# Performance work log

Hardware: AMD Instinct MI355X
Metric: run time of the kernel (lower is better)

Reference implementation:

```python
import jax, jax.numpy as jnp
import numpy as np
from jax import lax

L, B, H, Z, V = 64, 32, 256, 256, 32000  # steps, max_ast_depth, hidden=units, latent, vocab


def setup_inputs() -> dict:
    key = jax.random.key(0)
    ks = jax.random.split(key, 32)
    p = lambda i, shape: jax.random.normal(ks[i], shape, dtype=jnp.float32) * 0.05
    inp = {
        "nodes": jax.random.randint(ks[0], (L, B), 0, V),
        "edges": jax.random.randint(ks[1], (L, B), 0, 2) > 0,
        "enc_init": jax.random.normal(ks[2], (B, H), dtype=jnp.float32) * 0.001,
        "eps": jax.random.normal(ks[3], (B, Z), dtype=jnp.float32),
        "emb": p(4, (V, H)),
    }
    for j, n in enumerate(["enc_c", "enc_s", "dec_c", "dec_s"]):
        inp[n + "_Wih"] = p(5 + 4 * j, (3 * H, H))
        inp[n + "_Whh"] = p(6 + 4 * j, (3 * H, H))
        inp[n + "_bih"] = p(7 + 4 * j, (3 * H,))
        inp[n + "_bhh"] = p(8 + 4 * j, (3 * H,))
    inp["W_mean"] = p(21, (Z, H)); inp["b_mean"] = p(22, (Z,))
    inp["W_logv"] = p(23, (Z, H)); inp["b_logv"] = p(24, (Z,))
    inp["W_l2h"] = p(25, (H, Z)); inp["b_l2h"] = p(26, (H,))
    inp["W_voc"] = p(27, (V, H)); inp["b_voc"] = p(28, (V,))
    return inp


def _gru_cell(Wih, Whh, bih, bhh, x, h):
    # torch.nn.GRU single-layer cell; x, h: [B, H]
    gi = x @ Wih.T + bih
    gh = h @ Whh.T + bhh
    ir, iz, inn = jnp.split(gi, 3, axis=-1)
    hr, hz, hn = jnp.split(gh, 3, axis=-1)
    r = jax.nn.sigmoid(ir + hr)
    zg = jax.nn.sigmoid(iz + hz)
    n = jnp.tanh(inn + r * hn)
    return (1.0 - zg) * n + zg * h


def _tree_rnn(pc, ps, emb_nodes, edges, h0):
    # emb_nodes: [L, B, H], edges: [L, B] bool, h0: [B, H]
    # each step runs child & sibling GRUs on the SAME state, selects per node by edge
    def step(h, xe):
        x, e = xe
        hc = _gru_cell(*pc, x, h)
        hs = _gru_cell(*ps, x, h)
        h_new = jnp.where(e[:, None], hc, hs)
        return h_new, h_new  # 1-layer GRU, seq_len 1: output == new state
    h_final, outs = lax.scan(step, h0, (emb_nodes, edges))
    return outs, h_final  # outs: [L, B, H]


def reference(nodes, edges, enc_init, eps, emb,
              enc_c_Wih, enc_c_Whh, enc_c_bih, enc_c_bhh,
              enc_s_Wih, enc_s_Whh, enc_s_bih, enc_s_bhh,
              dec_c_Wih, dec_c_Whh, dec_c_bih, dec_c_bhh,
              dec_s_Wih, dec_s_Whh, dec_s_bih, dec_s_bhh,
              W_mean, b_mean, W_logv, b_logv, W_l2h, b_l2h, W_voc, b_voc):
    x = emb[nodes]  # [L, B, H]
    _, h_enc = _tree_rnn((enc_c_Wih, enc_c_Whh, enc_c_bih, enc_c_bhh),
                         (enc_s_Wih, enc_s_Whh, enc_s_bih, enc_s_bhh),
                         x, edges, enc_init)
    mean = h_enc @ W_mean.T + b_mean          # [B, Z]
    logv = h_enc @ W_logv.T + b_logv
    z = eps * jnp.exp(0.5 * logv) + mean      # reparameterization
    h0 = z @ W_l2h.T + b_l2h                  # decoder initial state [B, H]
    outs, _ = _tree_rnn((dec_c_Wih, dec_c_Whh, dec_c_bih, dec_c_bhh),
                        (dec_s_Wih, dec_s_Whh, dec_s_bih, dec_s_bhh),
                        x, edges, h0)         # [L, B, H]
    logits = outs @ W_voc.T + b_voc           # [L, B, V]
    logp = jax.nn.log_softmax(logits, axis=-1)
    return logp, mean, logv, z
```

## Files before the change

### kernel.cpp

```cpp
#include <hip/hip_runtime.h>
#include <stdint.h>

typedef unsigned short u16;
typedef unsigned int u32;

#define L_STEPS 64
#define B_SZ 32
#define H_SZ 256
#define Z_SZ 256
#define V_SZ 32000
#define H2 128
#define G3H 768

typedef _Float16 h2_t __attribute__((ext_vector_type(2)));
typedef _Float16 f16x8 __attribute__((ext_vector_type(8)));
typedef float f32x4 __attribute__((ext_vector_type(4)));

#define WHH2_OFF   0
#define WIH2_OFF   393216
#define WM2_OFF    786432
#define WLV2_OFF   819200
#define WL2H2_OFF  851968
#define GI2_OFF    884736
#define OUTS2_OFF  4030464
#define W16_OFF    4292608
#define WS_NEEDED  ((size_t)(W16_OFF + 4096000) * 4)

#define OUT_MEAN_OFF  65536000
#define OUT_LOGV_OFF  65544192
#define OUT_Z_OFF     65552384

__device__ __forceinline__ float fdot2(h2_t a, h2_t b, float c){
#if __has_builtin(__builtin_amdgcn_fdot2)
  return __builtin_amdgcn_fdot2(a, b, c, false);
#else
  return c + (float)a.x*(float)b.x + (float)a.y*(float)b.y;
#endif
}
__device__ __forceinline__ float sigm(float x){ return 1.f/(1.f + __expf(-x)); }

struct PackTArgs { const float2* src[11]; int n_h2[11]; int dstoff[11]; };

__global__ __launch_bounds__(256) void k_packt(PackTArgs p, h2_t* wsh){
  int m = blockIdx.y;
  int r = blockIdx.x*256 + threadIdx.x;
  if (r >= p.n_h2[m]) return;
  int row = r >> 7, k2 = r & 127;
  float2 f = p.src[m][r];
  h2_t h; h.x = (_Float16)f.x; h.y = (_Float16)f.y;
  int off = (((row>>6)*32 + (k2>>2))*64 + (row&63))*4 + (k2&3);
  wsh[p.dstoff[m] + off] = h;
}

__global__ __launch_bounds__(256) void k_packv(const float2* __restrict__ src,
                                               h2_t* __restrict__ dst, int total){
  int idx = blockIdx.x*256 + threadIdx.x;
  if (idx >= total) return;
  float2 f = src[idx];
  h2_t h; h.x = (_Float16)f.x; h.y = (_Float16)f.y;
  dst[idx] = h;
}

struct GiArgs { const float* bih[4]; };

__global__ __launch_bounds__(256) void k_gi(const int* __restrict__ nodes,
                                            const float* __restrict__ emb,
                                            const h2_t* __restrict__ wih2,
                                            GiArgs ga, h2_t* __restrict__ gi2){
  int l = blockIdx.x, g = blockIdx.y, t = threadIdx.x;
  __shared__ __align__(16) h2_t x2[B_SZ*132];
  #pragma unroll
  for (int it=0; it<16; ++it){
    int lin = it*256 + t;
    int bb = lin >> 7, k2 = lin & 127;
    int node = nodes[l*B_SZ + bb];
    float2 f = ((const float2*)(emb + (size_t)node*H_SZ))[k2];
    h2_t r; r.x=(_Float16)f.x; r.y=(_Float16)f.y;
    x2[bb*132 + k2] = r;
  }
  __syncthreads();
  const float* bih = ga.bih[g];
  for (int jc=0; jc<3; ++jc){
    int j = jc*256 + t;
    float acc[32];
    #pragma unroll
    for (int bb=0;bb<32;bb++) acc[bb]=0.f;
    const float4* Wv = (const float4*)wih2 + (size_t)g*24576 + (j>>6)*2048 + (j&63);
    #pragma unroll 2
    for (int kb=0;kb<32;kb++){
      union{float4 f; h2_t h[4];} w4;
      w4.f = Wv[kb*64];
      #pragma unroll
      for (int kc=0;kc<4;kc++){
        h2_t w = w4.h[kc];
        int k2 = kb*4 + kc;
        #pragma unroll
        for (int bb=0;bb<32;bb++) acc[bb] = fdot2(x2[bb*132+k2], w, acc[bb]);
      }
    }
    float bvv = bih[j];
    int base = (g*2048 + l*B_SZ)*384 + (j>>1);
    #pragma unroll
    for (int bb=0;bb<32;bb++){
      float own = acc[bb] + bvv;
      float oth = __shfl_xor(own, 1, 64);
      if (!(t&1)){
        h2_t r; r.x=(_Float16)own; r.y=(_Float16)oth;
        gi2[base + bb*384] = r;
      }
    }
  }
}

struct ScanArgs {
  const float* bhh[4];
  const float* b_mean; const float* b_logv; const float* b_l2h;
  const float* enc_init; const float* eps;
};

__global__ __launch_bounds__(768) void k_scan(const int* __restrict__ edges, ScanArgs sa,
                                              const h2_t* __restrict__ wsh,
                                              h2_t* __restrict__ outs2,
                                              float* __restrict__ out){
  int b = blockIdx.x, t = threadIdx.x;
  int i = t & 255, gate = t >> 8;
  int lane = t & 63, rb = t >> 6;
  __shared__ float h_lds[H_SZ];
  __shared__ __align__(16) h2_t hs2[H2];
  __shared__ float g_lds[512];
  __shared__ float s_bhh[4*G3H];
  __shared__ int s_edge[L_STEPS];
  const _Float16* gi_all = (const _Float16*)(wsh + GI2_OFF);

  if (t < H_SZ) h_lds[t] = sa.enc_init[b*H_SZ + t];
  if (t < L_STEPS) s_edge[t] = edges[t*B_SZ + b];
  #pragma unroll
  for (int m=0;m<4;m++) s_bhh[m*G3H + t] = sa.bhh[m][t];
  __syncthreads();
  if (t < H2){ h2_t r; r.x=(_Float16)h_lds[2*t]; r.y=(_Float16)h_lds[2*t+1]; hs2[t]=r; }
  __syncthreads();

  const float4* hsv = (const float4*)hs2;

  for (int ph=0; ph<2; ++ph){
    for (int l=0; l<L_STEPS; ++l){
      int e = s_edge[l];
      int gsel = (ph ? 2 : 0) + (e ? 0 : 1);
      float gi0=0.f, gi1=0.f, gi2v=0.f;
      if (t < H_SZ){
        const _Float16* gr = gi_all + (size_t)(gsel*2048 + l*B_SZ + b)*G3H;
        gi0  = (float)gr[i];
        gi1  = (float)gr[256+i];
        gi2v = (float)gr[512+i];
      }
      float bv = s_bhh[gsel*G3H + t];
      const float4* Wv = (const float4*)wsh + (size_t)gsel*24576 + rb*2048 + lane;
      float a0=0.f,a1=0.f,a2=0.f,a3=0.f;
      #pragma unroll 8
      for (int kb=0;kb<32;kb++){
        union{float4 f; h2_t h[4];} w, x;
        w.f = Wv[kb*64];
        x.f = hsv[kb];
        a0 = fdot2(x.h[0], w.h[0], a0);
        a1 = fdot2(x.h[1], w.h[1], a1);
        a2 = fdot2(x.h[2], w.h[2], a2);
        a3 = fdot2(x.h[3], w.h[3], a3);
      }
      float acc = (a0+a1)+(a2+a3) + bv;
      if (gate) g_lds[(gate-1)*256 + i] = acc;
      __syncthreads();
      if (t < H_SZ){
        float r = sigm(gi0 + acc);
        float z = sigm(gi1 + g_lds[i]);
        float n = tanhf(gi2v + r*g_lds[256+i]);
        float hn = (1.f - z)*n + z*h_lds[i];
        h_lds[i] = hn;
        float ho = __shfl_xor(hn, 1, 64);
        if (!(i & 1)){
          h2_t pk; pk.x=(_Float16)hn; pk.y=(_Float16)ho;
          hs2[i>>1] = pk;
          if (ph) outs2[(l*B_SZ + b)*H2 + (i>>1)] = pk;
        }
      }
      __syncthreads();
    }

    if (ph == 0){
      if (t < H_SZ){
        const float4* WmV = (const float4*)(wsh + WM2_OFF)  + (t>>6)*2048 + (t&63);
        const float4* WlV = (const float4*)(wsh + WLV2_OFF) + (t>>6)*2048 + (t&63);
        float m0=0.f,m1=0.f,m2=0.f,m3=0.f, l0=0.f,l1=0.f,l2=0.f,l3=0.f;
        #pragma unroll 8
        for (int kb=0;kb<32;kb++){
          union{float4 f; h2_t h[4];} wm, wl, x;
          x.f  = hsv[kb];
          wm.f = WmV[kb*64];
          wl.f = WlV[kb*64];
          m0=fdot2(x.h[0],wm.h[0],m0); m1=fdot2(x.h[1],wm.h[1],m1);
          m2=fdot2(x.h[2],wm.h[2],m2); m3=fdot2(x.h[3],wm.h[3],m3);
          l0=fdot2(x.h[0],wl.h[0],l0); l1=fdot2(x.h[1],wl.h[1],l1);
          l2=fdot2(x.h[2],wl.h[2],l2); l3=fdot2(x.h[3],wl.h[3],l3);
        }
        float am = (m0+m1)+(m2+m3) + sa.b_mean[t];
        float al = (l0+l1)+(l2+l3) + sa.b_logv[t];
        float zv = sa.eps[b*Z_SZ + t] * __expf(0.5f*al) + am;
        out[OUT_MEAN_OFF + b*Z_SZ + t] = am;
        out[OUT_LOGV_OFF + b*Z_SZ + t] = al;
        out[OUT_Z_OFF    + b*Z_SZ + t] = zv;
        h_lds[t] = zv;
      }
      __syncthreads();
      if (t < H2){ h2_t r; r.x=(_Float16)h_lds[2*t]; r.y=(_Float16)h_lds[2*t+1]; hs2[t]=r; }
      __syncthreads();
      float h0v = 0.f;
      if (t < H_SZ){
        const float4* WzV = (const float4*)(wsh + WL2H2_OFF) + (t>>6)*2048 + (t&63);
        float z0=0.f,z1=0.f,z2=0.f,z3=0.f;
        #pragma unroll 8
        for (int kb=0;kb<32;kb++){
          union{float4 f; h2_t h[4];} w, x;
          x.f = hsv[kb];
          w.f = WzV[kb*64];
          z0=fdot2(x.h[0],w.h[0],z0); z1=fdot2(x.h[1],w.h[1],z1);
          z2=fdot2(x.h[2],w.h[2],z2); z3=fdot2(x.h[3],w.h[3],z3);
        }
        h0v = (z0+z1)+(z2+z3) + sa.b_l2h[t];
      }
      __syncthreads();
      if (t < H_SZ) h_lds[t] = h0v;
      __syncthreads();
      if (t < H2){ h2_t r; r.x=(_Float16)h_lds[2*t]; r.y=(_Float16)h_lds[2*t+1]; hs2[t]=r; }
      __syncthreads();
    }
  }
}

__global__ __launch_bounds__(256) void k_gemm2(const h2_t* __restrict__ outs2,
                                               const _Float16* __restrict__ wv16,
                                               const float* __restrict__ bvoc,
                                               float* __restrict__ outf){
  int t = threadIdx.x;
  int lane = t & 63, w = t >> 6;
  int wm = w & 1, wn = w >> 1;
  int Mb = blockIdx.x * 64, Nb = blockIdx.y * 128;
  int lr = lane & 15, lq = lane >> 4;

  __shared__ __align__(16) _Float16 As[64*64];
  __shared__ __align__(16) _Float16 Bs[128*64];

  f32x4 acc[2][4];
  #pragma unroll
  for (int mi=0;mi<2;mi++)
    #pragma unroll
    for (int nj=0;nj<4;nj++) acc[mi][nj] = (f32x4){0.f,0.f,0.f,0.f};

  for (int kc=0; kc<4; ++kc){
    #pragma unroll
    for (int q=0;q<2;q++){
      int ch = q*256 + t;
      int row = ch >> 3, kb = ch & 7;
      float4 d = ((const float4*)(outs2 + (size_t)(Mb + row)*H2 + kc*32))[kb];
      ((float4*)As)[row*8 + (kb ^ (row & 7))] = d;
    }
    #pragma unroll
    for (int q=0;q<4;q++){
      int ch = q*256 + t;
      int row = ch >> 3, kb = ch & 7;
      float4 d = ((const float4*)(wv16 + (size_t)(Nb + row)*H_SZ + kc*64))[kb];
      ((float4*)Bs)[row*8 + (kb ^ (row & 7))] = d;
    }
    __syncthreads();
    union{float4 f; f16x8 h;} af[2][2], bf[4][2];
    #pragma unroll
    for (int mi=0;mi<2;mi++)
      #pragma unroll
      for (int kk=0;kk<2;kk++){
        int row = wm*32 + mi*16 + lr;
        int ks = kk*4 + lq;
        af[mi][kk].f = ((const float4*)As)[row*8 + (ks ^ (row & 7))];
      }
    #pragma unroll
    for (int nj=0;nj<4;nj++)
      #pragma unroll
      for (int kk=0;kk<2;kk++){
        int row = wn*64 + nj*16 + lr;
        int ks = kk*4 + lq;
        bf[nj][kk].f = ((const float4*)Bs)[row*8 + (ks ^ (row & 7))];
      }
    #pragma unroll
    for (int kk=0;kk<2;kk++)
      #pragma unroll
      for (int mi=0;mi<2;mi++)
        #pragma unroll
        for (int nj=0;nj<4;nj++)
          acc[mi][nj] = __builtin_amdgcn_mfma_f32_16x16x32_f16(
                          af[mi][kk].h, bf[nj][kk].h, acc[mi][nj], 0, 0, 0);
    __syncthreads();
  }

  #pragma unroll
  for (int nj=0;nj<4;nj++){
    int col = Nb + wn*64 + nj*16 + lr;
    float bias = bvoc[col];
    #pragma unroll
    for (int mi=0;mi<2;mi++){
      int r0 = Mb + wm*32 + mi*16 + lq*4;
      #pragma unroll
      for (int rg=0;rg<4;rg++)
        outf[(size_t)(r0 + rg)*V_SZ + col] = acc[mi][nj][rg] + bias;
    }
  }
}

__global__ __launch_bounds__(512) void k_gemm(const h2_t* __restrict__ outs2,
                                              const float* __restrict__ wv,
                                              const float* __restrict__ bvoc,
                                              float* __restrict__ outf){
  int t = threadIdx.x;
  int vq = t & 31, rq = t >> 5;
  int Nb = blockIdx.x * 256, Mb = blockIdx.y * 128;
  __shared__ __align__(16) h2_t A[16*128];
  __shared__ __align__(16) h2_t Bss[16*256];
  float acc[8][8];
  #pragma unroll
  for (int a=0;a<8;a++){
    #pragma unroll
    for (int c=0;c<8;c++) acc[a][c]=0.f;
  }

  for (int kc=0;kc<8;kc++){
    {
      int r = t >> 2, q = t & 3;
      union{float4 f; h2_t h[4];} u;
      u.f = ((const float4*)(outs2 + (Mb + r)*H2 + kc*16))[q];
      #pragma unroll
      for (int uu=0; uu<4; ++uu) A[(q*4+uu)*128 + r] = u.h[uu];
    }
    {
      int v = t >> 1, q = t & 1;
      const float* wrow = wv + (size_t)(Nb + v)*H_SZ + kc*32 + q*16;
      #pragma unroll
      for (int p=0;p<4;p++){
        float4 f = ((const float4*)wrow)[p];
        h2_t h0; h0.x=(_Float16)f.x; h0.y=(_Float16)f.y;
        h2_t h1; h1.x=(_Float16)f.z; h1.y=(_Float16)f.w;
        Bss[(q*8+p*2  )*256 + v] = h0;
        Bss[(q*8+p*2+1)*256 + v] = h1;
      }
    }
    __syncthreads();
    #pragma unroll 2
    for (int k2=0;k2<16;k2++){
      union{float4 f; h2_t h[4];} a0, a1, b0, b1;
      a0.f = *(const float4*)(A  + k2*128 + rq*8);
      a1.f = *(const float4*)(A  + k2*128 + rq*8 + 4);
      b0.f = *(const float4*)(Bss + k2*256 + vq*4);
      b1.f = *(const float4*)(Bss + k2*256 + vq*4 + 128);
      #pragma unroll
      for (int ii=0;ii<8;ii++){
        h2_t av = (ii<4)? a0.h[ii] : a1.h[ii-4];
        #pragma unroll
        for (int jj=0;jj<8;jj++){
          h2_t bv = (jj<4)? b0.h[jj] : b1.h[jj-4];
          acc[ii][jj] = fdot2(av, bv, acc[ii][jj]);
        }
      }
    }
    __syncthreads();
  }

  float bias0[4], bias1[4];
  #pragma unroll
  for (int jj=0;jj<4;jj++){
    bias0[jj] = bvoc[Nb + 4*vq + jj];
    bias1[jj] = bvoc[Nb + 128 + 4*vq + jj];
  }
  #pragma unroll
  for (int ii=0;ii<8;ii++){
    size_t base = (size_t)(Mb + rq*8 + ii)*(size_t)V_SZ + (size_t)Nb;
    float4 o0, o1;
    o0.x = acc[ii][0]+bias0[0]; o0.y = acc[ii][1]+bias0[1];
    o0.z = acc[ii][2]+bias0[2]; o0.w = acc[ii][3]+bias0[3];
    o1.x = acc[ii][4]+bias1[0]; o1.y = acc[ii][5]+bias1[1];
    o1.z = acc[ii][6]+bias1[2]; o1.w = acc[ii][7]+bias1[3];
    *(float4*)(outf + base + 4*vq)       = o0;
    *(float4*)(outf + base + 128 + 4*vq) = o1;
  }
}

__global__ __launch_bounds__(256) void k_softmax(float* __restrict__ outf){
  int rrow = blockIdx.x, t = threadIdx.x;
  float4* row = (float4*)(outf + (size_t)rrow * V_SZ);
  float4 v[32];
  #pragma unroll
  for (int i=0;i<31;i++) v[i] = row[i*256 + t];
  if (t < 64) v[31] = row[7936 + t];
  else { v[31].x = -1e30f; v[31].y = -1e30f; v[31].z = -1e30f; v[31].w = -1e30f; }

  float m = -1e30f;
  #pragma unroll
  for (int i=0;i<32;i++) m = fmaxf(m, fmaxf(fmaxf(v[i].x, v[i].y), fmaxf(v[i].z, v[i].w)));

  __shared__ float sred[4];
  __shared__ float sbc;
  int wid = t >> 6, lane = t & 63;
  #pragma unroll
  for (int o=32;o;o>>=1) m = fmaxf(m, __shfl_xor(m, o, 64));
  if (lane==0) sred[wid] = m;
  __syncthreads();
  if (t==0) sbc = fmaxf(fmaxf(sred[0],sred[1]), fmaxf(sred[2],sred[3]));
  __syncthreads();
  m = sbc;
  __syncthreads();

  float s = 0.f;
  #pragma unroll
  for (int i=0;i<32;i++){
    s += __expf(v[i].x - m) + __expf(v[i].y - m) + __expf(v[i].z - m) + __expf(v[i].w - m);
  }
  #pragma unroll
  for (int o=32;o;o>>=1) s += __shfl_xor(s, o, 64);
  if (lane==0) sred[wid] = s;
  __syncthreads();
  if (t==0) sbc = sred[0]+sred[1]+sred[2]+sred[3];
  __syncthreads();
  float lse = m + logf(sbc);

  #pragma unroll
  for (int i=0;i<31;i++){
    v[i].x -= lse; v[i].y -= lse; v[i].z -= lse; v[i].w -= lse;
    row[i*256 + t] = v[i];
  }
  if (t < 64){
    v[31].x -= lse; v[31].y -= lse; v[31].z -= lse; v[31].w -= lse;
    row[7936 + t] = v[31];
  }
}

extern "C" void kernel_launch(void* const* d_in, const int* in_sizes, int n_in,
                              void* d_out, int out_size, void* d_ws, size_t ws_size,
                              hipStream_t stream){
  const int* nodes = (const int*)d_in[0];
  const int* edges = (const int*)d_in[1];
  h2_t* wsh = (h2_t*)d_ws;
  float* outf = (float*)d_out;
  bool mfma_path = (ws_size >= WS_NEEDED);

  PackTArgs pt;
  const int srcidx[11] = {6,10,14,18, 5,9,13,17, 21,23,25};
  for (int k=0;k<11;k++){
    pt.src[k] = (const float2*)d_in[srcidx[k]];
    pt.n_h2[k] = (k < 8) ? 98304 : 32768;
  }
  for (int k=0;k<4;k++) pt.dstoff[k]   = WHH2_OFF + k*98304;
  for (int k=0;k<4;k++) pt.dstoff[4+k] = WIH2_OFF + k*98304;
  pt.dstoff[8] = WM2_OFF; pt.dstoff[9] = WLV2_OFF; pt.dstoff[10] = WL2H2_OFF;
  k_packt<<<dim3(384,11), dim3(256), 0, stream>>>(pt, wsh);

  if (mfma_path)
    k_packv<<<dim3(16000), dim3(256), 0, stream>>>((const float2*)d_in[27],
                                                   wsh + W16_OFF, 4096000);

  GiArgs ga;
  ga.bih[0]=(const float*)d_in[7];  ga.bih[1]=(const float*)d_in[11];
  ga.bih[2]=(const float*)d_in[15]; ga.bih[3]=(const float*)d_in[19];
  k_gi<<<dim3(64,4), dim3(256), 0, stream>>>(nodes, (const float*)d_in[4], wsh + WIH2_OFF, ga, wsh + GI2_OFF);

  ScanArgs sa;
  sa.bhh[0]=(const float*)d_in[8];  sa.bhh[1]=(const float*)d_in[12];
  sa.bhh[2]=(const float*)d_in[16]; sa.bhh[3]=(const float*)d_in[20];
  sa.b_mean=(const float*)d_in[22]; sa.b_logv=(const float*)d_in[24]; sa.b_l2h=(const float*)d_in[26];
  sa.enc_init=(const float*)d_in[2]; sa.eps=(const float*)d_in[3];
  k_scan<<<dim3(32), dim3(768), 0, stream>>>(edges, sa, wsh, wsh + OUTS2_OFF, outf);

  if (mfma_path)
    k_gemm2<<<dim3(32,250), dim3(256), 0, stream>>>(wsh + OUTS2_OFF,
                                                    (const _Float16*)(wsh + W16_OFF),
                                                    (const float*)d_in[28], outf);
  else
    k_gemm<<<dim3(125,16), dim3(512), 0, stream>>>(wsh + OUTS2_OFF, (const float*)d_in[27],
                                                   (const float*)d_in[28], outf);

  k_softmax<<<dim3(2048), dim3(256), 0, stream>>>(outf);
}
```

Before: 971.2 us.

## Compute log-sum-exp in a separate GEMM pass and fuse normalization into logits write

Instead of writing raw logits (a 2048x32000 fp32 array) and then reading and rewriting it in a separate softmax kernel, a first MFMA pass computes per-row partial online max/sum over column slices. A small reduction turns these into per-row LSE values, and the main GEMM then writes logits minus LSE directly. This trades the two extra full passes over the large output for recomputing the GEMM once. It also software-pipelines the weight loads in the scan's recurrent matvec with double-buffered register arrays.

```diff
diff --git a/kernel.cpp b/kernel.cpp
--- a/kernel.cpp
+++ b/kernel.cpp
@@ -25,6 +25,8 @@
 #define OUTS2_OFF  4030464
 #define W16_OFF    4292608
 #define WS_NEEDED  ((size_t)(W16_OFF + 4096000) * 4)
+
+#define NPART 20
 
 #define OUT_MEAN_OFF  65536000
 #define OUT_LOGV_OFF  65544192
@@ -156,15 +158,28 @@
       float bv = s_bhh[gsel*G3H + t];
       const float4* Wv = (const float4*)wsh + (size_t)gsel*24576 + rb*2048 + lane;
       float a0=0.f,a1=0.f,a2=0.f,a3=0.f;
-      #pragma unroll 8
-      for (int kb=0;kb<32;kb++){
-        union{float4 f; h2_t h[4];} w, x;
-        w.f = Wv[kb*64];
-        x.f = hsv[kb];
-        a0 = fdot2(x.h[0], w.h[0], a0);
-        a1 = fdot2(x.h[1], w.h[1], a1);
-        a2 = fdot2(x.h[2], w.h[2], a2);
-        a3 = fdot2(x.h[3], w.h[3], a3);
+      float4 wa[8], wb[8];
+      #pragma unroll
+      for (int j=0;j<8;j++) wa[j] = Wv[j*64];
+      #pragma unroll
+      for (int c=0;c<4;c++){
+        float4* cur = (c&1)? wb : wa;
+        float4* nxt = (c&1)? wa : wb;
+        if (c<3){
+          const float4* Wn = Wv + (size_t)(c+1)*512;
+          #pragma unroll
+          for (int j=0;j<8;j++) nxt[j] = Wn[j*64];
+        }
+        #pragma unroll
+        for (int j=0;j<8;j++){
+          union{float4 f; h2_t h[4];} w, x;
+          w.f = cur[j];
+          x.f = hsv[c*8+j];
+          a0 = fdot2(x.h[0], w.h[0], a0);
+          a1 = fdot2(x.h[1], w.h[1], a1);
+          a2 = fdot2(x.h[2], w.h[2], a2);
+          a3 = fdot2(x.h[3], w.h[3], a3);
+        }
       }
       float acc = (a0+a1)+(a2+a3) + bv;
       if (gate) g_lds[(gate-1)*256 + i] = acc;
@@ -235,9 +250,120 @@
   }
 }
 
-__global__ __launch_bounds__(256) void k_gemm2(const h2_t* __restrict__ outs2,
+__global__ __launch_bounds__(256) void k_lse(const h2_t* __restrict__ outs2,
+                                             const _Float16* __restrict__ wv16,
+                                             const float* __restrict__ bvoc,
+                                             float* __restrict__ part){
+  int t = threadIdx.x;
+  int lane = t & 63, w = t >> 6;
+  int wm = w & 1, wn = w >> 1;
+  int Mb = blockIdx.x * 64, ns = blockIdx.y;
+  int lr = lane & 15, lq = lane >> 4;
+
+  __shared__ __align__(16) float4 As4[4*64*8];
+
+  #pragma unroll
+  for (int q=0;q<8;q++){
+    int c = q*256 + t;
+    int kc = c >> 9, row = (c >> 3) & 63, kb = c & 7;
+    float4 d = ((const float4*)(outs2 + (size_t)(Mb+row)*H2))[kc*8 + kb];
+    As4[kc*512 + row*8 + (kb ^ (row & 7))] = d;
+  }
+  __syncthreads();
+
+  union{float4 f; f16x8 h;} af[4][2][2];
+  #pragma unroll
+  for (int kc=0;kc<4;kc++)
+    #pragma unroll
+    for (int mi=0;mi<2;mi++)
+      #pragma unroll
+      for (int kk=0;kk<2;kk++){
+        int row = wm*32 + mi*16 + lr;
+        af[kc][mi][kk].f = As4[kc*512 + row*8 + ((kk*4+lq) ^ (row&7))];
+      }
+
+  float mrun[2][4], srun[2][4];
+  #pragma unroll
+  for (int mi=0;mi<2;mi++)
+    #pragma unroll
+    for (int rg=0;rg<4;rg++){ mrun[mi][rg] = -1e30f; srun[mi][rg] = 0.f; }
+
+  for (int nb=0; nb<25; ++nb){
+    int col0 = ns*3200 + nb*128 + wn*64;
+    f32x4 acc[2][4];
+    #pragma unroll
+    for (int mi=0;mi<2;mi++)
+      #pragma unroll
+      for (int nj=0;nj<4;nj++) acc[mi][nj] = (f32x4){0.f,0.f,0.f,0.f};
+
+    float bias[4];
+    #pragma unroll
+    for (int nj=0;nj<4;nj++){
+      int col = col0 + nj*16 + lr;
+      bias[nj] = bvoc[col];
+      const float4* bp = (const float4*)(wv16 + (size_t)col*H_SZ);
+      #pragma unroll
+      for (int kc=0;kc<4;kc++)
+        #pragma unroll
+        for (int kk=0;kk<2;kk++){
+          union{float4 f; f16x8 h;} bf;
+          bf.f = bp[kc*8 + kk*4 + lq];
+          #pragma unroll
+          for (int mi=0;mi<2;mi++)
+            acc[mi][nj] = __builtin_amdgcn_mfma_f32_16x16x32_f16(
+                            af[kc][mi][kk].h, bf.h, acc[mi][nj], 0, 0, 0);
+        }
+    }
+    #pragma unroll
+    for (int mi=0;mi<2;mi++)
+      #pragma unroll
+      for (int rg=0;rg<4;rg++){
+        float v0 = acc[mi][0][rg] + bias[0];
+        float v1 = acc[mi][1][rg] + bias[1];
+        float v2 = acc[mi][2][rg] + bias[2];
+        float v3 = acc[mi][3][rg] + bias[3];
+        float mx = fmaxf(fmaxf(v0,v1), fmaxf(v2,v3));
+        #pragma unroll
+        for (int o=1;o<16;o<<=1) mx = fmaxf(mx, __shfl_xor(mx, o, 64));
+        float sv = __expf(v0-mx)+__expf(v1-mx)+__expf(v2-mx)+__expf(v3-mx);
+        #pragma unroll
+        for (int o=1;o<16;o<<=1) sv += __shfl_xor(sv, o, 64);
+        float nm = fmaxf(mrun[mi][rg], mx);
+        srun[mi][rg] = srun[mi][rg]*__expf(mrun[mi][rg]-nm) + sv*__expf(mx-nm);
+        mrun[mi][rg] = nm;
+      }
+  }
+
+  if (lr == 0){
+    #pragma unroll
+    for (int mi=0;mi<2;mi++)
+      #pragma unroll
+      for (int rg=0;rg<4;rg++){
+        int row = Mb + wm*32 + mi*16 + lq*4 + rg;
+        int p = ns*2 + wn;
+        part[(row*NPART + p)*2 + 0] = mrun[mi][rg];
+        part[(row*NPART + p)*2 + 1] = srun[mi][rg];
+      }
+  }
+}
+
+__global__ __launch_bounds__(256) void k_lsered(const float* __restrict__ part,
+                                                float* __restrict__ lse){
+  int r = blockIdx.x*256 + threadIdx.x;
+  if (r >= 2048) return;
+  float M = -1e30f;
+  #pragma unroll
+  for (int p=0;p<NPART;p++) M = fmaxf(M, part[(r*NPART+p)*2]);
+  float S = 0.f;
+  #pragma unroll
+  for (int p=0;p<NPART;p++) S += part[(r*NPART+p)*2+1] * __expf(part[(r*NPART+p)*2] - M);
+  lse[r] = M + logf(S);
+}
+
+__global__ __launch_bounds__(256) void k_gemm3(const h2_t* __restrict__ outs2,
                                                const _Float16* __restrict__ wv16,
                                                const float* __restrict__ bvoc,
+                                               const float* __restrict__ lse,
                                                float* __restrict__ outf){
   int t = threadIdx.x;
   int lane = t & 63, w = t >> 6;
@@ -299,15 +425,18 @@
   }
 
   #pragma unroll
-  for (int nj=0;nj<4;nj++){
-    int col = Nb + wn*64 + nj*16 + lr;
-    float bias = bvoc[col];
-    #pragma unroll
-    for (int mi=0;mi<2;mi++){
-      int r0 = Mb + wm*32 + mi*16 + lq*4;
+  for (int mi=0;mi<2;mi++){
+    int r0 = Mb + wm*32 + mi*16 + lq*4;
+    float lsev[4];
+    #pragma unroll
+    for (int rg=0;rg<4;rg++) lsev[rg] = lse[r0+rg];
+    #pragma unroll
+    for (int nj=0;nj<4;nj++){
+      int col = Nb + wn*64 + nj*16 + lr;
+      float bias = bvoc[col];
       #pragma unroll
       for (int rg=0;rg<4;rg++)
-        outf[(size_t)(r0 + rg)*V_SZ + col] = acc[mi][nj][rg] + bias;
+        outf[(size_t)(r0 + rg)*V_SZ + col] = acc[mi][nj][rg] + bias - lsev[rg];
     }
   }
 }
@@ -473,13 +602,19 @@
   sa.enc_init=(const float*)d_in[2]; sa.eps=(const float*)d_in[3];
   k_scan<<<dim3(32), dim3(768), 0, stream>>>(edges, sa, wsh, wsh + OUTS2_OFF, outf);
 
-  if (mfma_path)
-    k_gemm2<<<dim3(32,250), dim3(256), 0, stream>>>(wsh + OUTS2_OFF,
+  if (mfma_path){
+    float* part = (float*)(wsh + GI2_OFF);
+    float* lse  = part + 2048*NPART*2;
+    k_lse<<<dim3(32,10), dim3(256), 0, stream>>>(wsh + OUTS2_OFF,
+                                                 (const _Float16*)(wsh + W16_OFF),
+                                                 (const float*)d_in[28], part);
+    k_lsered<<<dim3(8), dim3(256), 0, stream>>>(part, lse);
+    k_gemm3<<<dim3(32,250), dim3(256), 0, stream>>>(wsh + OUTS2_OFF,
                                                     (const _Float16*)(wsh + W16_OFF),
-                                                    (const float*)d_in[28], outf);
-  else
+                                                    (const float*)d_in[28], lse, outf);
+  } else {
     k_gemm<<<dim3(125,16), dim3(512), 0, stream>>>(wsh + OUTS2_OFF, (const float*)d_in[27],
                                                    (const float*)d_in[28], outf);
-
-  k_softmax<<<dim3(2048), dim3(256), 0, stream>>>(outf);
-}
+    k_softmax<<<dim3(2048), dim3(256), 0, stream>>>(outf);
+  }
+}
```

Result: slower. 1.160 ms (+19.4%).

## Fuse log-softmax max/sum partials into vocab GEMM epilogue

Applied to the files above, without the earlier changes.

The vocab GEMM epilogue now computes per-row partial max and sum-exp for each N tile and writes them to a workspace. A small reduction kernel combines the partials into a per-row log-sum-exp, and a final pass subtracts it from the logits in place. This replaces the standalone softmax kernel and is meant to remove one full pass over the large logits tensor. It adds shuffle and exp work to the GEMM epilogue and an extra serial-ish reduction launch.

```diff
diff --git a/kernel.cpp b/kernel.cpp
--- a/kernel.cpp
+++ b/kernel.cpp
@@ -25,6 +25,8 @@
 #define OUTS2_OFF  4030464
 #define W16_OFF    4292608
 #define WS_NEEDED  ((size_t)(W16_OFF + 4096000) * 4)
+
+#define NPART 250
 
 #define OUT_MEAN_OFF  65536000
 #define OUT_LOGV_OFF  65544192
@@ -235,10 +237,11 @@
   }
 }
 
-__global__ __launch_bounds__(256) void k_gemm2(const h2_t* __restrict__ outs2,
+__global__ __launch_bounds__(256) void k_gemmS(const h2_t* __restrict__ outs2,
                                                const _Float16* __restrict__ wv16,
                                                const float* __restrict__ bvoc,
-                                               float* __restrict__ outf){
+                                               float* __restrict__ outf,
+                                               float* __restrict__ part){
   int t = threadIdx.x;
   int lane = t & 63, w = t >> 6;
   int wm = w & 1, wn = w >> 1;
@@ -247,6 +250,7 @@
 
   __shared__ __align__(16) _Float16 As[64*64];
   __shared__ __align__(16) _Float16 Bs[128*64];
+  __shared__ float red[2][64][2];
 
   f32x4 acc[2][4];
   #pragma unroll
@@ -298,17 +302,66 @@
     __syncthreads();
   }
 
-  #pragma unroll
-  for (int nj=0;nj<4;nj++){
-    int col = Nb + wn*64 + nj*16 + lr;
-    float bias = bvoc[col];
-    #pragma unroll
-    for (int mi=0;mi<2;mi++){
-      int r0 = Mb + wm*32 + mi*16 + lq*4;
-      #pragma unroll
-      for (int rg=0;rg<4;rg++)
-        outf[(size_t)(r0 + rg)*V_SZ + col] = acc[mi][nj][rg] + bias;
-    }
+  float bias[4];
+  #pragma unroll
+  for (int nj=0;nj<4;nj++) bias[nj] = bvoc[Nb + wn*64 + nj*16 + lr];
+  #pragma unroll
+  for (int mi=0;mi<2;mi++){
+    int r0 = Mb + wm*32 + mi*16 + lq*4;
+    #pragma unroll
+    for (int rg=0;rg<4;rg++){
+      float v[4];
+      #pragma unroll
+      for (int nj=0;nj<4;nj++){
+        v[nj] = acc[mi][nj][rg] + bias[nj];
+        outf[(size_t)(r0 + rg)*V_SZ + (Nb + wn*64 + nj*16 + lr)] = v[nj];
+      }
+      float mx = fmaxf(fmaxf(v[0],v[1]), fmaxf(v[2],v[3]));
+      #pragma unroll
+      for (int o=1;o<16;o<<=1) mx = fmaxf(mx, __shfl_xor(mx, o, 64));
+      float sv = __expf(v[0]-mx)+__expf(v[1]-mx)+__expf(v[2]-mx)+__expf(v[3]-mx);
+      #pragma unroll
+      for (int o=1;o<16;o<<=1) sv += __shfl_xor(sv, o, 64);
+      if (lr == 0){
+        int rloc = wm*32 + mi*16 + lq*4 + rg;
+        red[wn][rloc][0] = mx;
+        red[wn][rloc][1] = sv;
+      }
+    }
+  }
+  __syncthreads();
+  if (t < 64){
+    float m0 = red[0][t][0], s0 = red[0][t][1];
+    float m1 = red[1][t][0], s1 = red[1][t][1];
+    float M = fmaxf(m0, m1);
+    float S = s0*__expf(m0-M) + s1*__expf(m1-M);
+    int row = Mb + t;
+    part[((size_t)row*NPART + blockIdx.y)*2 + 0] = M;
+    part[((size_t)row*NPART + blockIdx.y)*2 + 1] = S;
+  }
+}
+
+__global__ __launch_bounds__(256) void k_lsered(const float* __restrict__ part,
+                                                float* __restrict__ lse){
+  int r = blockIdx.x*256 + threadIdx.x;
+  if (r >= 2048) return;
+  const float* pr = part + (size_t)r*NPART*2;
+  float M = -1e30f;
+  for (int p=0;p<NPART;p++) M = fmaxf(M, pr[p*2]);
+  float S = 0.f;
+  for (int p=0;p<NPART;p++) S += pr[p*2+1] * __expf(pr[p*2] - M);
+  lse[r] = M + logf(S);
+}
+
+__global__ __launch_bounds__(256) void k_final(float* __restrict__ outf,
+                                               const float* __restrict__ lse){
+  int r = blockIdx.x;
+  float l = lse[r];
+  float4* row = (float4*)(outf + (size_t)r * V_SZ);
+  for (int c = threadIdx.x; c < 8000; c += 256){
+    float4 v = row[c];
+    v.x -= l; v.y -= l; v.z -= l; v.w -= l;
+    row[c] = v;
   }
 }
 
@@ -473,13 +526,17 @@
   sa.enc_init=(const float*)d_in[2]; sa.eps=(const float*)d_in[3];
   k_scan<<<dim3(32), dim3(768), 0, stream>>>(edges, sa, wsh, wsh + OUTS2_OFF, outf);
 
-  if (mfma_path)
-    k_gemm2<<<dim3(32,250), dim3(256), 0, stream>>>(wsh + OUTS2_OFF,
+  if (mfma_path){
+    float* part = (float*)(wsh + GI2_OFF);
+    float* lse  = part + 2048*NPART*2;
+    k_gemmS<<<dim3(32,250), dim3(256), 0, stream>>>(wsh + OUTS2_OFF,
                                                     (const _Float16*)(wsh + W16_OFF),
-                                                    (const float*)d_in[28], outf);
-  else
+                                                    (const float*)d_in[28], outf, part);
+    k_lsered<<<dim3(8), dim3(256), 0, stream>>>(part, lse);
+    k_final<<<dim3(2048), dim3(256), 0, stream>>>(outf, lse);
+  } else {
     k_gemm<<<dim3(125,16), dim3(512), 0, stream>>>(wsh + OUTS2_OFF, (const float*)d_in[27],
                                                    (const float*)d_in[28], outf);
-
-  k_softmax<<<dim3(2048), dim3(256), 0, stream>>>(outf);
-}
+    k_softmax<<<dim3(2048), dim3(256), 0, stream>>>(outf);
+  }
+}
```

Result: slower. 1.053 ms (+8.5%).
